# Optimization experiments

Measured on AMD Instinct MI355X. Metric: run time of the kernel, lower is better.

The kernel has to match this reference:

```python
import jax, jax.numpy as jnp
import numpy as np
from jax import lax

TAU = 1.0  # registered buffer, default 1.0 -> Q_tau = +inf -> clamp is a no-op
EPS = 1e-5
SQRT2 = float(np.sqrt(2.0))

# sign with straight-through estimator (weights): grad = identity
@jax.custom_vjp
def sign_w(w):
    return jnp.sign(w)
def _sign_w_fwd(w):
    return jnp.sign(w), None
def _sign_w_bwd(_, g):
    return (g,)
sign_w.defvjp(_sign_w_fwd, _sign_w_bwd)

@jax.custom_vjp
def sign_a(x):
    return jnp.sign(x)
def _sign_a_fwd(x):
    return jnp.sign(x), x
def _sign_a_bwd(x, g):
    return (jnp.maximum(2.0 - jnp.abs(2.0 * x), 0.0) * g,)
sign_a.defvjp(_sign_a_fwd, _sign_a_bwd)

def binarize_conv2d(a, w, alpha, stride=1):
    # weight standardization (torch.var is unbiased -> ddof=1)
    w0 = w - jnp.mean(w, axis=(1, 2, 3), keepdims=True)
    var = jnp.var(w0, axis=(1, 2, 3), keepdims=True, ddof=1)
    w1 = w0 * (2.0 * SQRT2) / jnp.sqrt(var + EPS)
    EW = jnp.mean(jnp.abs(w1))
    Q_tau = lax.stop_gradient(-EW * jnp.log(2.0 - 2.0 * TAU))  # +inf for tau=1
    w2 = jnp.clip(w1, -Q_tau, Q_tau)
    bw = sign_w(w2)
    ba = sign_a(a)  # eval mode: a0 = a (no per-sample var normalization)
    out = lax.conv_general_dilated(
        ba, bw, window_strides=(stride, stride), padding=((1, 1), (1, 1)),
        dimension_numbers=('NCHW', 'OIHW', 'NCHW'))
    return out * alpha[None]  # alpha: [C_out,1,1] -> broadcast over N,H,W

def bn_eval(x, gamma, beta, mean, var):
    scale = (gamma / jnp.sqrt(var + EPS)).reshape(1, -1, 1, 1)
    shift = (beta - mean * gamma / jnp.sqrt(var + EPS)).reshape(1, -1, 1, 1)
    return x * scale + shift

def hardtanh(x):
    return jnp.clip(x, -1.0, 1.0)

def setup_inputs() -> dict:
    key = jax.random.key(0)
    ks = jax.random.split(key, 13)
    N, C, H, W = 64, 256, 32, 32
    return {
        'x': jax.random.normal(ks[0], (N, C, H, W), jnp.float32),
        'conv1_w': jax.random.normal(ks[1], (C, C, 3, 3), jnp.float32) * 0.05,
        'alpha1': jax.random.uniform(ks[2], (C, 1, 1), jnp.float32),
        'bn1_gamma': jax.random.uniform(ks[3], (C,), jnp.float32) + 0.5,
        'bn1_beta': jax.random.normal(ks[4], (C,), jnp.float32) * 0.1,
        'bn1_mean': jax.random.normal(ks[5], (C,), jnp.float32),
        'bn1_var': jax.random.uniform(ks[6], (C,), jnp.float32) + 0.5,
        'conv2_w': jax.random.normal(ks[7], (C, C, 3, 3), jnp.float32) * 0.05,
        'alpha2': jax.random.uniform(ks[8], (C, 1, 1), jnp.float32),
        'bn2_gamma': jax.random.uniform(ks[9], (C,), jnp.float32) + 0.5,
        'bn2_beta': jax.random.normal(ks[10], (C,), jnp.float32) * 0.1,
        'bn2_mean': jax.random.normal(ks[11], (C,), jnp.float32),
        'bn2_var': jax.random.uniform(ks[12], (C,), jnp.float32) + 0.5,
    }

def reference(x, conv1_w, alpha1, bn1_gamma, bn1_beta, bn1_mean, bn1_var,
              conv2_w, alpha2, bn2_gamma, bn2_beta, bn2_mean, bn2_var):
    out = hardtanh(bn_eval(binarize_conv2d(x, conv1_w, alpha1, stride=1),
                           bn1_gamma, bn1_beta, bn1_mean, bn1_var))
    out = bn_eval(binarize_conv2d(out, conv2_w, alpha2, stride=1),
                  bn2_gamma, bn2_beta, bn2_mean, bn2_var)
    out = out + x  # identity shortcut (stride=1, in_planes==planes)
    return hardtanh(out)
```

## Files before the change

### kernel.cpp

```cpp
#include <hip/hip_runtime.h>
#include <cstdint>
#include <cstddef>

using u32 = unsigned int;
using u64 = unsigned long long;

typedef int v4i  __attribute__((ext_vector_type(4)));
typedef int v16i __attribute__((ext_vector_type(16)));

#define EPSV 1e-5f
#define MFMA_I8(A, B, C) __builtin_amdgcn_mfma_i32_32x32x32_i8((A), (B), (C), 0, 0, 0)

__global__ void prep_weights(const float* __restrict__ w1, const float* __restrict__ w2,
                             const float* __restrict__ a1, const float* __restrict__ g1,
                             const float* __restrict__ b1, const float* __restrict__ m1,
                             const float* __restrict__ v1,
                             const float* __restrict__ a2, const float* __restrict__ g2,
                             const float* __restrict__ b2, const float* __restrict__ m2,
                             const float* __restrict__ v2,
                             unsigned char* __restrict__ Wsgn, float4* __restrict__ SC4)
{
    const int co   = blockIdx.x;
    const int conv = blockIdx.y;
    const int c    = threadIdx.x;
    const float* w = conv ? w2 : w1;

    float wv[9];
    const float* wp = w + ((size_t)co * 256 + c) * 9;
    float s = 0.f;
#pragma unroll
    for (int p = 0; p < 9; ++p) { wv[p] = wp[p]; s += wv[p]; }

    __shared__ float red[256];
    red[c] = s;
    __syncthreads();
    for (int off = 128; off > 0; off >>= 1) {
        if (c < off) red[c] += red[c + off];
        __syncthreads();
    }
    const float mean = __fdiv_rn(red[0], 2304.0f);

    unsigned char* wrow = Wsgn + ((size_t)(conv * 256 + co) * 9) * 256;
#pragma unroll
    for (int p = 0; p < 9; ++p)
        wrow[p * 256 + c] = (wv[p] > mean) ? 0x01u : 0xFFu;

    if (c == 0) {
        const float alpha = conv ? a2[co] : a1[co];
        const float gamma = conv ? g2[co] : g1[co];
        const float beta  = conv ? b2[co] : b1[co];
        const float mu    = conv ? m2[co] : m1[co];
        const float var   = conv ? v2[co] : v1[co];
        const float sq    = __fsqrt_rn(__fadd_rn(var, EPSV));
        const float scale = __fdiv_rn(gamma, sq);
        const float shift = __fsub_rn(beta, __fdiv_rn(__fmul_rn(mu, gamma), sq));
        SC4[conv * 256 + co] = make_float4(alpha, scale, shift, 0.f);
    }
}

__global__ void build_bfrag(const unsigned char* __restrict__ Wsgn, uint4* __restrict__ Bf)
{
    const int f    = blockIdx.x;
    const int lane = threadIdx.x;
    const int conv = f / 576;
    const int rem  = f % 576;
    const int g    = rem / 72;
    const int p    = (rem % 72) / 8;
    const int cb   = rem % 8;
    const int co   = g * 32 + (lane & 31);
    const unsigned char* src = Wsgn + ((size_t)(conv * 256 + co) * 9 + p) * 256
                                    + cb * 32 + (lane >> 5) * 16;
    Bf[(size_t)f * 64 + lane] = *(const uint4*)src;
}

__global__ void binarize_x(const float* __restrict__ x, u32* __restrict__ A1)
{
    const int n = blockIdx.x >> 3;
    const int j = blockIdx.x & 7;
    const int p = threadIdx.x;
    const float* xp = x + (((size_t)n * 256 + j * 32) * 1024) + p;
    u32 bits = 0;
#pragma unroll
    for (int k = 0; k < 32; ++k) {
        float v = xp[(size_t)k * 1024];
        bits |= (v > 0.f ? 1u : 0u) << k;
    }
    A1[((size_t)n * 1024 + p) * 8 + j] = bits;
}

__device__ __forceinline__ u32 expand4(u32 x)
{
    u32 r;
    r  = ((x & 1u) ? 0x00000001u : 0x000000FFu);
    r |= ((x & 2u) ? 0x00000100u : 0x0000FF00u);
    r |= ((x & 4u) ? 0x00010000u : 0x00FF0000u);
    r |= ((x & 8u) ? 0x01000000u : 0xFF000000u);
    return r;
}

__device__ __forceinline__ void glds16(const void* g, void* l)
{
    __builtin_amdgcn_global_load_lds(
        (const __attribute__((address_space(1))) void*)g,
        (__attribute__((address_space(3))) void*)l, 16, 0, 0);
}

template<int CONV>
__global__ __launch_bounds__(512, 2)
void conv_mfma(const u32* __restrict__ A_in, const v4i* __restrict__ Bf,
               const float4* __restrict__ SC4, const float* __restrict__ X,
               u32* __restrict__ A_out, float* __restrict__ OUT)
{
    const int n    = blockIdx.x >> 2;
    const int yo   = blockIdx.x & 3;
    const int y0   = yo * 8;
    const int tid  = threadIdx.x;
    const int wave = tid >> 6;
    const int lane = tid & 63;
    const int wm   = wave >> 2;
    const int wn   = wave & 3;
    const int col0 = lane & 31;
    const int g0   = wn * 2;

    __shared__ alignas(16) unsigned char lds[103424];

    const int fbias = (CONV == 2) ? 576 : 0;
    const char* bsrcA = (const char*)Bf + (((size_t)(fbias + g0 * 72)) << 10)
                        + (size_t)lane * 16;
    const char* bsrcB = bsrcA + (72u << 10);
    unsigned char* bdst = lds + 87040 + (size_t)g0 * 1024;

    glds16(bsrcA,        bdst);
    glds16(bsrcB,        bdst + 1024);
    glds16(bsrcA + 1024, bdst + 8192);
    glds16(bsrcB + 1024, bdst + 8192 + 1024);

    for (int s = tid; s < 5440; s += 512) {
        const int colv = s % 34;
        const int rest = s / 34;
        const int r    = rest % 10;
        const int c16  = rest / 10;
        const int iy   = y0 - 1 + r;
        const int ix   = colv - 1;
        u32 d0 = 0, d1 = 0, d2 = 0, d3 = 0;
        if ((unsigned)iy < 32u && (unsigned)ix < 32u) {
            const u32 wrd = A_in[((size_t)n * 1024 + iy * 32 + ix) * 8 + (c16 >> 1)];
            const u32 h = (wrd >> ((c16 & 1) * 16)) & 0xFFFFu;
            d0 = expand4(h);
            d1 = expand4(h >> 4);
            d2 = expand4(h >> 8);
            d3 = expand4(h >> 12);
        }
        *(uint4*)(lds + (size_t)s * 16) = make_uint4(d0, d1, d2, d3);
    }

    const int bias2 = (CONV == 2) ? 256 : 0;
    const float4 scA = SC4[bias2 + (g0 + 0) * 32 + col0];
    const float4 scB = SC4[bias2 + (g0 + 1) * 32 + col0];

    __syncthreads();

    const v16i Z  = {0,0,0,0,0,0,0,0,0,0,0,0,0,0,0,0};
    v16i c0a = Z, c0b = Z, c1a = Z, c1b = Z;
    v16i c2a = Z, c2b = Z, c3a = Z, c3b = Z;

    const u32 lc16off = (u32)((lane >> 5) * 5440);
    const u32 rowbase = (u32)((4 * wm) * 544);
    const u32 bwoff   = (u32)(g0 * 1024 + lane * 16);

    v4i ea0, ea1, ea2, ea3, eb0, eb1;
    v4i oa0, oa1, oa2, oa3, ob0, ob1;
    {
        const u32 ao = lc16off + rowbase + (u32)(col0 * 16);
        ea0 = *(const v4i*)(lds + ao);
        ea1 = *(const v4i*)(lds + ao + 544);
        ea2 = *(const v4i*)(lds + ao + 1088);
        ea3 = *(const v4i*)(lds + ao + 1632);
        const u32 bo = 87040u + bwoff;
        eb0 = *(const v4i*)(lds + bo);
        eb1 = *(const v4i*)(lds + bo + 1024);
    }

#define PHASE(KC, AN0, AN1, AN2, AN3, BN0, BN1, AC0, AC1, AC2, AC3, BC0, BC1)   \
    {                                                                           \
        const int k_ = (KC);                                                    \
        int kf_ = k_ + 2; if (kf_ >= 72) kf_ -= 72;                             \
        {                                                                       \
            unsigned char* d_ = bdst + ((k_ & 1) << 13);                        \
            glds16(bsrcA + ((size_t)kf_ << 10), d_);                            \
            glds16(bsrcB + ((size_t)kf_ << 10), d_ + 1024);                     \
        }                                                                       \
        __builtin_amdgcn_sched_barrier(0);                                      \
        {                                                                       \
            const int kn_ = k_ + 1;                                             \
            const int cb_ = kn_ & 7, p_ = kn_ >> 3;                             \
            const int dy_ = p_ / 3, dx_ = p_ - dy_ * 3;                         \
            const u32 ao_ = lc16off + (u32)(2 * cb_) * 5440u + rowbase          \
                          + (u32)(dy_ * 544) + (u32)((dx_ + col0) * 16);        \
            AN0 = *(const v4i*)(lds + ao_);                                     \
            AN1 = *(const v4i*)(lds + ao_ + 544);                               \
            AN2 = *(const v4i*)(lds + ao_ + 1088);                              \
            AN3 = *(const v4i*)(lds + ao_ + 1632);                              \
            asm volatile("s_waitcnt vmcnt(2)" ::: "memory");                    \
            __builtin_amdgcn_sched_barrier(0);                                  \
            const u32 bo_ = 87040u + (u32)((kn_ & 1) << 13) + bwoff;            \
            BN0 = *(const v4i*)(lds + bo_);                                     \
            BN1 = *(const v4i*)(lds + bo_ + 1024);                              \
        }                                                                       \
        __builtin_amdgcn_s_barrier();                                           \
        asm volatile("s_waitcnt lgkmcnt(6)" ::: "memory");                      \
        __builtin_amdgcn_sched_barrier(0);                                      \
        __builtin_amdgcn_s_setprio(1);                                          \
        c0a = MFMA_I8(AC0, BC0, c0a);  c0b = MFMA_I8(AC0, BC1, c0b);            \
        c1a = MFMA_I8(AC1, BC0, c1a);  c1b = MFMA_I8(AC1, BC1, c1b);            \
        c2a = MFMA_I8(AC2, BC0, c2a);  c2b = MFMA_I8(AC2, BC1, c2b);            \
        c3a = MFMA_I8(AC3, BC0, c3a);  c3b = MFMA_I8(AC3, BC1, c3b);            \
        __builtin_amdgcn_s_setprio(0);                                          \
        __builtin_amdgcn_s_barrier();                                           \
    }

#pragma unroll 1
    for (int j = 0; j < 36; ++j) {
        const int k = j * 2;
        PHASE(k,     oa0, oa1, oa2, oa3, ob0, ob1,  ea0, ea1, ea2, ea3, eb0, eb1)
        PHASE(k + 1, ea0, ea1, ea2, ea3, eb0, eb1,  oa0, oa1, oa2, oa3, ob0, ob1)
    }
#undef PHASE

    if (CONV == 1) {
#define EP1(ACC, MR, GI, SC)                                                    \
        { _Pragma("unroll")                                                     \
          for (int reg = 0; reg < 16; ++reg) {                                  \
              const float t = __fadd_rn(__fmul_rn(__fmul_rn((float)ACC[reg],    \
                                        SC.x), SC.y), SC.z);                    \
              const u64 m = __ballot(t > 0.f);                                  \
              if (lane == 0) {                                                  \
                  const int x = (reg & 3) + 8 * (reg >> 2);                     \
                  const int row = y0 + 4 * wm + (MR);                           \
                  const size_t pb = (size_t)n * 1024 + row * 32 + x;            \
                  A_out[pb * 8 + (g0 + (GI))]       = (u32)m;                   \
                  A_out[(pb + 4) * 8 + (g0 + (GI))] = (u32)(m >> 32);           \
              } } }
        EP1(c0a, 0, 0, scA)  EP1(c0b, 0, 1, scB)
        EP1(c1a, 1, 0, scA)  EP1(c1b, 1, 1, scB)
        EP1(c2a, 2, 0, scA)  EP1(c2b, 2, 1, scB)
        EP1(c3a, 3, 0, scA)  EP1(c3b, 3, 1, scB)
#undef EP1
    } else {
        __syncthreads();
        float* ep = (float*)lds;
#define EP2PASS(CA, CB, R)                                                      \
        { if (wm == ((R) >> 2)) {                                               \
            _Pragma("unroll")                                                   \
            for (int reg = 0; reg < 16; ++reg) {                                \
                const int x = (reg & 3) + 8 * (reg >> 2) + 4 * (lane >> 5);     \
                ep[x * 257 + (g0 + 0) * 32 + col0] =                            \
                    __fadd_rn(__fmul_rn(__fmul_rn((float)CA[reg], scA.x),       \
                                        scA.y), scA.z);                         \
                ep[x * 257 + (g0 + 1) * 32 + col0] =                            \
                    __fadd_rn(__fmul_rn(__fmul_rn((float)CB[reg], scB.x),       \
                                        scB.y), scB.z);                         \
            } }                                                                 \
          __syncthreads();                                                      \
          {                                                                     \
              const int co = tid >> 1, xh = tid & 1;                            \
              const size_t gb = ((size_t)(n * 256 + co)) * 1024                 \
                              + (y0 + (R)) * 32 + xh * 16;                      \
              _Pragma("unroll")                                                 \
              for (int x4 = 0; x4 < 16; x4 += 4) {                              \
                  float4 rr;                                                    \
                  rr.x = ep[(xh * 16 + x4 + 0) * 257 + co];                     \
                  rr.y = ep[(xh * 16 + x4 + 1) * 257 + co];                     \
                  rr.z = ep[(xh * 16 + x4 + 2) * 257 + co];                     \
                  rr.w = ep[(xh * 16 + x4 + 3) * 257 + co];                     \
                  const float4 xv = *(const float4*)(X + gb + x4);              \
                  rr.x = fminf(1.f, fmaxf(-1.f, __fadd_rn(rr.x, xv.x)));        \
                  rr.y = fminf(1.f, fmaxf(-1.f, __fadd_rn(rr.y, xv.y)));        \
                  rr.z = fminf(1.f, fmaxf(-1.f, __fadd_rn(rr.z, xv.z)));        \
                  rr.w = fminf(1.f, fmaxf(-1.f, __fadd_rn(rr.w, xv.w)));        \
                  *(float4*)(OUT + gb + x4) = rr;                               \
              }                                                                 \
          }                                                                     \
          __syncthreads(); }
        EP2PASS(c0a, c0b, 0)
        EP2PASS(c1a, c1b, 1)
        EP2PASS(c2a, c2b, 2)
        EP2PASS(c3a, c3b, 3)
        EP2PASS(c0a, c0b, 4)
        EP2PASS(c1a, c1b, 5)
        EP2PASS(c2a, c2b, 6)
        EP2PASS(c3a, c3b, 7)
#undef EP2PASS
    }
}

extern "C" void kernel_launch(void* const* d_in, const int* in_sizes, int n_in,
                              void* d_out, int out_size, void* d_ws, size_t ws_size,
                              hipStream_t stream)
{
    const float* x   = (const float*)d_in[0];
    const float* w1  = (const float*)d_in[1];
    const float* al1 = (const float*)d_in[2];
    const float* g1  = (const float*)d_in[3];
    const float* b1  = (const float*)d_in[4];
    const float* m1  = (const float*)d_in[5];
    const float* v1  = (const float*)d_in[6];
    const float* w2  = (const float*)d_in[7];
    const float* al2 = (const float*)d_in[8];
    const float* g2  = (const float*)d_in[9];
    const float* b2  = (const float*)d_in[10];
    const float* m2  = (const float*)d_in[11];
    const float* v2  = (const float*)d_in[12];
    float* out = (float*)d_out;

    char* ws = (char*)d_ws;
    float4*        SC4  = (float4*)(ws);
    unsigned char* Wsgn = (unsigned char*)(ws + (64u << 10));
    uint4*         Bf   = (uint4*)(ws + (2u << 20));
    u32*           A1   = (u32*)(ws + (4u << 20));
    u32*           A2   = (u32*)(ws + (6u << 20));
    (void)ws_size; (void)in_sizes; (void)n_in; (void)out_size;

    prep_weights<<<dim3(256, 2), 256, 0, stream>>>(w1, w2, al1, g1, b1, m1, v1,
                                                   al2, g2, b2, m2, v2, Wsgn, SC4);
    build_bfrag<<<dim3(1152), 64, 0, stream>>>(Wsgn, Bf);
    binarize_x<<<dim3(512), 1024, 0, stream>>>(x, A1);
    conv_mfma<1><<<dim3(256), 512, 0, stream>>>(A1, (const v4i*)Bf, SC4,
                                                nullptr, A2, nullptr);
    conv_mfma<2><<<dim3(256), 512, 0, stream>>>(A2, (const v4i*)Bf, SC4,
                                                x, nullptr, out);
}
```

Baseline: 129.9 us.

## Use 4 waves with 4x4 MFMA tiles per wave and per-wave B pipeline

```diff
diff --git a/kernel.cpp b/kernel.cpp
--- a/kernel.cpp
+++ b/kernel.cpp
@@ -106,7 +106,7 @@
 }
 
 template<int CONV>
-__global__ __launch_bounds__(512, 2)
+__global__ __launch_bounds__(256, 1)
 void conv_mfma(const u32* __restrict__ A_in, const v4i* __restrict__ Bf,
                const float4* __restrict__ SC4, const float* __restrict__ X,
                u32* __restrict__ A_out, float* __restrict__ OUT)
@@ -117,25 +117,30 @@
     const int tid  = threadIdx.x;
     const int wave = tid >> 6;
     const int lane = tid & 63;
-    const int wm   = wave >> 2;
-    const int wn   = wave & 3;
+    const int wm   = wave >> 1;
+    const int wn   = wave & 1;
     const int col0 = lane & 31;
-    const int g0   = wn * 2;
-
-    __shared__ alignas(16) unsigned char lds[103424];
+    const int g0   = wn * 4;
+
+    __shared__ alignas(16) unsigned char lds[152576];
 
     const int fbias = (CONV == 2) ? 576 : 0;
-    const char* bsrcA = (const char*)Bf + (((size_t)(fbias + g0 * 72)) << 10)
-                        + (size_t)lane * 16;
-    const char* bsrcB = bsrcA + (72u << 10);
-    unsigned char* bdst = lds + 87040 + (size_t)g0 * 1024;
-
-    glds16(bsrcA,        bdst);
-    glds16(bsrcB,        bdst + 1024);
-    glds16(bsrcA + 1024, bdst + 8192);
-    glds16(bsrcB + 1024, bdst + 8192 + 1024);
-
-    for (int s = tid; s < 5440; s += 512) {
+    const char* bs0 = (const char*)Bf + (((size_t)(fbias + (g0 + 0) * 72)) << 10) + (size_t)lane * 16;
+    const char* bs1 = (const char*)Bf + (((size_t)(fbias + (g0 + 1) * 72)) << 10) + (size_t)lane * 16;
+    const char* bs2 = (const char*)Bf + (((size_t)(fbias + (g0 + 2) * 72)) << 10) + (size_t)lane * 16;
+    const char* bs3 = (const char*)Bf + (((size_t)(fbias + (g0 + 3) * 72)) << 10) + (size_t)lane * 16;
+    unsigned char* bdst = lds + 87040 + (size_t)wave * 16384;
+
+#pragma unroll
+    for (int s = 0; s < 3; ++s) {
+        unsigned char* d = bdst + s * 4096;
+        glds16(bs0 + ((size_t)s << 10), d);
+        glds16(bs1 + ((size_t)s << 10), d + 1024);
+        glds16(bs2 + ((size_t)s << 10), d + 2048);
+        glds16(bs3 + ((size_t)s << 10), d + 3072);
+    }
+
+    for (int s = tid; s < 5440; s += 256) {
         const int colv = s % 34;
         const int rest = s / 34;
         const int r    = rest % 10;
@@ -157,78 +162,92 @@
     const int bias2 = (CONV == 2) ? 256 : 0;
     const float4 scA = SC4[bias2 + (g0 + 0) * 32 + col0];
     const float4 scB = SC4[bias2 + (g0 + 1) * 32 + col0];
+    const float4 scC = SC4[bias2 + (g0 + 2) * 32 + col0];
+    const float4 scD = SC4[bias2 + (g0 + 3) * 32 + col0];
 
     __syncthreads();
 
     const v16i Z  = {0,0,0,0,0,0,0,0,0,0,0,0,0,0,0,0};
-    v16i c0a = Z, c0b = Z, c1a = Z, c1b = Z;
-    v16i c2a = Z, c2b = Z, c3a = Z, c3b = Z;
-
-    const u32 lc16off = (u32)((lane >> 5) * 5440);
-    const u32 rowbase = (u32)((4 * wm) * 544);
-    const u32 bwoff   = (u32)(g0 * 1024 + lane * 16);
-
-    v4i ea0, ea1, ea2, ea3, eb0, eb1;
-    v4i oa0, oa1, oa2, oa3, ob0, ob1;
+    v16i c00 = Z, c01 = Z, c02 = Z, c03 = Z;
+    v16i c10 = Z, c11 = Z, c12 = Z, c13 = Z;
+    v16i c20 = Z, c21 = Z, c22 = Z, c23 = Z;
+    v16i c30 = Z, c31 = Z, c32 = Z, c33 = Z;
+
+    const u32 lhalf = (u32)((lane >> 5) * 5440);
+    const u32 bb    = 87040u + (u32)(wave * 16384 + lane * 16);
+
+    v4i ea0, ea1, ea2, ea3, eb0, eb1, eb2, eb3;
+    v4i oa0, oa1, oa2, oa3, ob0, ob1, ob2, ob3;
     {
-        const u32 ao = lc16off + rowbase + (u32)(col0 * 16);
+        const u32 ao = (lhalf + (u32)((4 * wm) * 544 + col0 * 16)) * 16u / 16u;
         ea0 = *(const v4i*)(lds + ao);
+        ea1 = *(const v4i*)(lds + ao + 544 * 16 / 16 * 1 + 544 - 544 + 544);
         ea1 = *(const v4i*)(lds + ao + 544);
         ea2 = *(const v4i*)(lds + ao + 1088);
         ea3 = *(const v4i*)(lds + ao + 1632);
-        const u32 bo = 87040u + bwoff;
-        eb0 = *(const v4i*)(lds + bo);
-        eb1 = *(const v4i*)(lds + bo + 1024);
-    }
-
-#define PHASE(KC, AN0, AN1, AN2, AN3, BN0, BN1, AC0, AC1, AC2, AC3, BC0, BC1)   \
+        eb0 = *(const v4i*)(lds + bb);
+        eb1 = *(const v4i*)(lds + bb + 1024);
+        eb2 = *(const v4i*)(lds + bb + 2048);
+        eb3 = *(const v4i*)(lds + bb + 3072);
+    }
+
+#define SB __builtin_amdgcn_sched_barrier(0)
+
+#define STEP(KC, A0,A1,A2,A3, B0,B1,B2,B3, NA0,NA1,NA2,NA3, NB0,NB1,NB2,NB3)    \
     {                                                                           \
         const int k_ = (KC);                                                    \
-        int kf_ = k_ + 2; if (kf_ >= 72) kf_ -= 72;                             \
-        {                                                                       \
-            unsigned char* d_ = bdst + ((k_ & 1) << 13);                        \
-            glds16(bsrcA + ((size_t)kf_ << 10), d_);                            \
-            glds16(bsrcB + ((size_t)kf_ << 10), d_ + 1024);                     \
+        asm volatile("s_waitcnt lgkmcnt(0)" ::: "memory");                      \
+        SB;                                                                     \
+        {    \
+            int kg = k_ + 3; if (kg >= 72) kg -= 72;                            \
+            unsigned char* d_ = bdst + ((k_ + 3) & 3) * 4096;                   \
+            glds16(bs0 + ((size_t)kg << 10), d_);                               \
+            glds16(bs1 + ((size_t)kg << 10), d_ + 1024);                        \
+            glds16(bs2 + ((size_t)kg << 10), d_ + 2048);                        \
+            glds16(bs3 + ((size_t)kg << 10), d_ + 3072);                        \
         }                                                                       \
-        __builtin_amdgcn_sched_barrier(0);                                      \
-        {                                                                       \
-            const int kn_ = k_ + 1;                                             \
-            const int cb_ = kn_ & 7, p_ = kn_ >> 3;                             \
-            const int dy_ = p_ / 3, dx_ = p_ - dy_ * 3;                         \
-            const u32 ao_ = lc16off + (u32)(2 * cb_) * 5440u + rowbase          \
-                          + (u32)(dy_ * 544) + (u32)((dx_ + col0) * 16);        \
-            AN0 = *(const v4i*)(lds + ao_);                                     \
-            AN1 = *(const v4i*)(lds + ao_ + 544);                               \
-            AN2 = *(const v4i*)(lds + ao_ + 1088);                              \
-            AN3 = *(const v4i*)(lds + ao_ + 1632);                              \
-            asm volatile("s_waitcnt vmcnt(2)" ::: "memory");                    \
-            __builtin_amdgcn_sched_barrier(0);                                  \
-            const u32 bo_ = 87040u + (u32)((kn_ & 1) << 13) + bwoff;            \
-            BN0 = *(const v4i*)(lds + bo_);                                     \
-            BN1 = *(const v4i*)(lds + bo_ + 1024);                              \
-        }                                                                       \
-        __builtin_amdgcn_s_barrier();                                           \
-        asm volatile("s_waitcnt lgkmcnt(6)" ::: "memory");                      \
-        __builtin_amdgcn_sched_barrier(0);                                      \
-        __builtin_amdgcn_s_setprio(1);                                          \
-        c0a = MFMA_I8(AC0, BC0, c0a);  c0b = MFMA_I8(AC0, BC1, c0b);            \
-        c1a = MFMA_I8(AC1, BC0, c1a);  c1b = MFMA_I8(AC1, BC1, c1b);            \
-        c2a = MFMA_I8(AC2, BC0, c2a);  c2b = MFMA_I8(AC2, BC1, c2b);            \
-        c3a = MFMA_I8(AC3, BC0, c3a);  c3b = MFMA_I8(AC3, BC1, c3b);            \
-        __builtin_amdgcn_s_setprio(0);                                          \
-        __builtin_amdgcn_s_barrier();                                           \
+        SB;                                                                     \
+        const int kn_ = k_ + 1;                                                 \
+        const int cbn_ = kn_ & 7, pn_ = kn_ >> 3;                               \
+        const int dyn_ = (pn_ * 11) >> 5;                                       \
+        const int dxn_ = pn_ - dyn_ * 3;                                        \
+        const u32 aon_ = lhalf + (u32)(cbn_ * 10880)                            \
+                       + (u32)((4 * wm + dyn_) * 544)                          \
+                       + (u32)((col0 + dxn_) * 16);                            \
+        const u32 bon_ = bb + (u32)((kn_ & 3) * 4096);                          \
+        NA0 = *(const v4i*)(lds + aon_);                                        \
+        c00 = MFMA_I8(A0, B0, c00);  c01 = MFMA_I8(A0, B1, c01);  SB;           \
+        NA1 = *(const v4i*)(lds + aon_ + 544);                                  \
+        c02 = MFMA_I8(A0, B2, c02);  c03 = MFMA_I8(A0, B3, c03);  SB;           \
+        NA2 = *(const v4i*)(lds + aon_ + 1088);                                 \
+        c10 = MFMA_I8(A1, B0, c10);  c11 = MFMA_I8(A1, B1, c11);  SB;           \
+        NA3 = *(const v4i*)(lds + aon_ + 1632);                                 \
+        c12 = MFMA_I8(A1, B2, c12);  c13 = MFMA_I8(A1, B3, c13);  SB;           \
+        asm volatile("s_waitcnt vmcnt(8)" ::: "memory");                        \
+        SB;                                                                     \
+        NB0 = *(const v4i*)(lds + bon_);                                        \
+        c20 = MFMA_I8(A2, B0, c20);  c21 = MFMA_I8(A2, B1, c21);  SB;           \
+        NB1 = *(const v4i*)(lds + bon_ + 1024);                                 \
+        c22 = MFMA_I8(A2, B2, c22);  c23 = MFMA_I8(A2, B3, c23);  SB;           \
+        NB2 = *(const v4i*)(lds + bon_ + 2048);                                 \
+        c30 = MFMA_I8(A3, B0, c30);  c31 = MFMA_I8(A3, B1, c31);  SB;           \
+        NB3 = *(const v4i*)(lds + bon_ + 3072);                                 \
+        c32 = MFMA_I8(A3, B2, c32);  c33 = MFMA_I8(A3, B3, c33);  SB;           \
     }
 
 #pragma unroll 1
     for (int j = 0; j < 36; ++j) {
         const int k = j * 2;
-        PHASE(k,     oa0, oa1, oa2, oa3, ob0, ob1,  ea0, ea1, ea2, ea3, eb0, eb1)
-        PHASE(k + 1, ea0, ea1, ea2, ea3, eb0, eb1,  oa0, oa1, oa2, oa3, ob0, ob1)
-    }
-#undef PHASE
+        STEP(k,     ea0,ea1,ea2,ea3, eb0,eb1,eb2,eb3,
+                    oa0,oa1,oa2,oa3, ob0,ob1,ob2,ob3)
+        STEP(k + 1, oa0,oa1,oa2,oa3, ob0,ob1,ob2,ob3,
+                    ea0,ea1,ea2,ea3, eb0,eb1,eb2,eb3)
+    }
+#undef STEP
+#undef SB
 
     if (CONV == 1) {
-#define EP1(ACC, MR, GI, SC)                                                    \
+#define EP1(ACC, RI, GI, SC)                                                    \
         { _Pragma("unroll")                                                     \
           for (int reg = 0; reg < 16; ++reg) {                                  \
               const float t = __fadd_rn(__fmul_rn(__fmul_rn((float)ACC[reg],    \
@@ -236,20 +255,20 @@
               const u64 m = __ballot(t > 0.f);                                  \
               if (lane == 0) {                                                  \
                   const int x = (reg & 3) + 8 * (reg >> 2);                     \
-                  const int row = y0 + 4 * wm + (MR);                           \
+                  const int row = y0 + 4 * wm + (RI);                           \
                   const size_t pb = (size_t)n * 1024 + row * 32 + x;            \
                   A_out[pb * 8 + (g0 + (GI))]       = (u32)m;                   \
                   A_out[(pb + 4) * 8 + (g0 + (GI))] = (u32)(m >> 32);           \
               } } }
-        EP1(c0a, 0, 0, scA)  EP1(c0b, 0, 1, scB)
-        EP1(c1a, 1, 0, scA)  EP1(c1b, 1, 1, scB)
-        EP1(c2a, 2, 0, scA)  EP1(c2b, 2, 1, scB)
-        EP1(c3a, 3, 0, scA)  EP1(c3b, 3, 1, scB)
+        EP1(c00, 0, 0, scA)  EP1(c01, 0, 1, scB)  EP1(c02, 0, 2, scC)  EP1(c03, 0, 3, scD)
+        EP1(c10, 1, 0, scA)  EP1(c11, 1, 1, scB)  EP1(c12, 1, 2, scC)  EP1(c13, 1, 3, scD)
+        EP1(c20, 2, 0, scA)  EP1(c21, 2, 1, scB)  EP1(c22, 2, 2, scC)  EP1(c23, 2, 3, scD)
+        EP1(c30, 3, 0, scA)  EP1(c31, 3, 1, scB)  EP1(c32, 3, 2, scC)  EP1(c33, 3, 3, scD)
 #undef EP1
     } else {
         __syncthreads();
         float* ep = (float*)lds;
-#define EP2PASS(CA, CB, R)                                                      \
+#define EP2PASS(CA, CB, CC, CD, R)                                              \
         { if (wm == ((R) >> 2)) {                                               \
             _Pragma("unroll")                                                   \
             for (int reg = 0; reg < 16; ++reg) {                                \
@@ -260,19 +279,25 @@
                 ep[x * 257 + (g0 + 1) * 32 + col0] =                            \
                     __fadd_rn(__fmul_rn(__fmul_rn((float)CB[reg], scB.x),       \
                                         scB.y), scB.z);                         \
+                ep[x * 257 + (g0 + 2) * 32 + col0] =                            \
+                    __fadd_rn(__fmul_rn(__fmul_rn((float)CC[reg], scC.x),       \
+                                        scC.y), scC.z);                         \
+                ep[x * 257 + (g0 + 3) * 32 + col0] =                            \
+                    __fadd_rn(__fmul_rn(__fmul_rn((float)CD[reg], scD.x),       \
+                                        scD.y), scD.z);                         \
             } }                                                                 \
           __syncthreads();                                                      \
           {                                                                     \
-              const int co = tid >> 1, xh = tid & 1;                            \
+              const int co = tid;                                               \
               const size_t gb = ((size_t)(n * 256 + co)) * 1024                 \
-                              + (y0 + (R)) * 32 + xh * 16;                      \
+                              + (y0 + (R)) * 32;                                \
               _Pragma("unroll")                                                 \
-              for (int x4 = 0; x4 < 16; x4 += 4) {                              \
+              for (int x4 = 0; x4 < 32; x4 += 4) {                              \
                   float4 rr;                                                    \
-                  rr.x = ep[(xh * 16 + x4 + 0) * 257 + co];                     \
-                  rr.y = ep[(xh * 16 + x4 + 1) * 257 + co];                     \
-                  rr.z = ep[(xh * 16 + x4 + 2) * 257 + co];                     \
-                  rr.w = ep[(xh * 16 + x4 + 3) * 257 + co];                     \
+                  rr.x = ep[(x4 + 0) * 257 + co];                               \
+                  rr.y = ep[(x4 + 1) * 257 + co];                               \
+                  rr.z = ep[(x4 + 2) * 257 + co];                               \
+                  rr.w = ep[(x4 + 3) * 257 + co];                               \
                   const float4 xv = *(const float4*)(X + gb + x4);              \
                   rr.x = fminf(1.f, fmaxf(-1.f, __fadd_rn(rr.x, xv.x)));        \
                   rr.y = fminf(1.f, fmaxf(-1.f, __fadd_rn(rr.y, xv.y)));        \
@@ -282,14 +307,14 @@
               }                                                                 \
           }                                                                     \
           __syncthreads(); }
-        EP2PASS(c0a, c0b, 0)
-        EP2PASS(c1a, c1b, 1)
-        EP2PASS(c2a, c2b, 2)
-        EP2PASS(c3a, c3b, 3)
-        EP2PASS(c0a, c0b, 4)
-        EP2PASS(c1a, c1b, 5)
-        EP2PASS(c2a, c2b, 6)
-        EP2PASS(c3a, c3b, 7)
+        EP2PASS(c00, c01, c02, c03, 0)
+        EP2PASS(c10, c11, c12, c13, 1)
+        EP2PASS(c20, c21, c22, c23, 2)
+        EP2PASS(c30, c31, c32, c33, 3)
+        EP2PASS(c00, c01, c02, c03, 4)
+        EP2PASS(c10, c11, c12, c13, 5)
+        EP2PASS(c20, c21, c22, c23, 6)
+        EP2PASS(c30, c31, c32, c33, 7)
 #undef EP2PASS
     }
 }
@@ -325,8 +350,8 @@
                                                    al2, g2, b2, m2, v2, Wsgn, SC4);
     build_bfrag<<<dim3(1152), 64, 0, stream>>>(Wsgn, Bf);
     binarize_x<<<dim3(512), 1024, 0, stream>>>(x, A1);
-    conv_mfma<1><<<dim3(256), 512, 0, stream>>>(A1, (const v4i*)Bf, SC4,
+    conv_mfma<1><<<dim3(256), 256, 0, stream>>>(A1, (const v4i*)Bf, SC4,
                                                 nullptr, A2, nullptr);
-    conv_mfma<2><<<dim3(256), 512, 0, stream>>>(A2, (const v4i*)Bf, SC4,
+    conv_mfma<2><<<dim3(256), 256, 0, stream>>>(A2, (const v4i*)Bf, SC4,
                                                 x, nullptr, out);
 }
```

Result: slower. 310.5 us (+139.2%).

## Process two K-steps per barrier phase with a 4-deep weight ring and XCD block swizzle

Applied to the files above, without the earlier changes.

```diff
diff --git a/kernel.cpp b/kernel.cpp
--- a/kernel.cpp
+++ b/kernel.cpp
@@ -111,8 +111,9 @@
                const float4* __restrict__ SC4, const float* __restrict__ X,
                u32* __restrict__ A_out, float* __restrict__ OUT)
 {
-    const int n    = blockIdx.x >> 2;
-    const int yo   = blockIdx.x & 3;
+    const int logical = (blockIdx.x & 7) * 32 + (blockIdx.x >> 3);
+    const int n    = logical >> 2;
+    const int yo   = logical & 3;
     const int y0   = yo * 8;
     const int tid  = threadIdx.x;
     const int wave = tid >> 6;
@@ -122,18 +123,23 @@
     const int col0 = lane & 31;
     const int g0   = wn * 2;
 
-    __shared__ alignas(16) unsigned char lds[103424];
+    __shared__ alignas(16) unsigned char lds[152576];
 
     const int fbias = (CONV == 2) ? 576 : 0;
     const char* bsrcA = (const char*)Bf + (((size_t)(fbias + g0 * 72)) << 10)
                         + (size_t)lane * 16;
     const char* bsrcB = bsrcA + (72u << 10);
-    unsigned char* bdst = lds + 87040 + (size_t)g0 * 1024;
-
-    glds16(bsrcA,        bdst);
-    glds16(bsrcB,        bdst + 1024);
-    glds16(bsrcA + 1024, bdst + 8192);
-    glds16(bsrcB + 1024, bdst + 8192 + 1024);
+
+#pragma unroll
+    for (int pf = 0; pf < 2; ++pf) {
+        unsigned char* d = lds + 87040 + pf * 16384 + wn * 4096;
+        const size_t k0 = (size_t)(2 * pf) << 10;
+        const size_t k1 = (size_t)(2 * pf + 1) << 10;
+        glds16(bsrcA + k0, d);
+        glds16(bsrcB + k0, d + 1024);
+        glds16(bsrcA + k1, d + 2048);
+        glds16(bsrcB + k1, d + 3072);
+    }
 
     for (int s = tid; s < 5440; s += 512) {
         const int colv = s % 34;
@@ -164,66 +170,90 @@
     v16i c0a = Z, c0b = Z, c1a = Z, c1b = Z;
     v16i c2a = Z, c2b = Z, c3a = Z, c3b = Z;
 
-    const u32 lc16off = (u32)((lane >> 5) * 5440);
+    const u32 lhalf   = (u32)((lane >> 5) * 5440);
     const u32 rowbase = (u32)((4 * wm) * 544);
-    const u32 bwoff   = (u32)(g0 * 1024 + lane * 16);
-
-    v4i ea0, ea1, ea2, ea3, eb0, eb1;
-    v4i oa0, oa1, oa2, oa3, ob0, ob1;
+    const u32 bwoff   = (u32)(wn * 4096 + lane * 16);
+
+    v4i ea0, ea1, ea2, ea3, ea4, ea5, ea6, ea7;
+    v4i oa0, oa1, oa2, oa3, oa4, oa5, oa6, oa7;
     {
-        const u32 ao = lc16off + rowbase + (u32)(col0 * 16);
-        ea0 = *(const v4i*)(lds + ao);
-        ea1 = *(const v4i*)(lds + ao + 544);
-        ea2 = *(const v4i*)(lds + ao + 1088);
-        ea3 = *(const v4i*)(lds + ao + 1632);
-        const u32 bo = 87040u + bwoff;
-        eb0 = *(const v4i*)(lds + bo);
-        eb1 = *(const v4i*)(lds + bo + 1024);
-    }
-
-#define PHASE(KC, AN0, AN1, AN2, AN3, BN0, BN1, AC0, AC1, AC2, AC3, BC0, BC1)   \
+        const u32 a0 = lhalf + rowbase + (u32)(col0 * 16);
+        ea0 = *(const v4i*)(lds + a0);
+        ea1 = *(const v4i*)(lds + a0 + 544);
+        ea2 = *(const v4i*)(lds + a0 + 1088);
+        ea3 = *(const v4i*)(lds + a0 + 1632);
+        const u32 a1 = a0 + 10880;
+        ea4 = *(const v4i*)(lds + a1);
+        ea5 = *(const v4i*)(lds + a1 + 544);
+        ea6 = *(const v4i*)(lds + a1 + 1088);
+        ea7 = *(const v4i*)(lds + a1 + 1632);
+    }
+
+#define PHASE(PH, AC0,AC1,AC2,AC3,AC4,AC5,AC6,AC7,                              \
+                  AN0,AN1,AN2,AN3,AN4,AN5,AN6,AN7)                              \
     {                                                                           \
-        const int k_ = (KC);                                                    \
-        int kf_ = k_ + 2; if (kf_ >= 72) kf_ -= 72;                             \
-        {                                                                       \
-            unsigned char* d_ = bdst + ((k_ & 1) << 13);                        \
-            glds16(bsrcA + ((size_t)kf_ << 10), d_);                            \
-            glds16(bsrcB + ((size_t)kf_ << 10), d_ + 1024);                     \
+        const int ph_ = (PH);                                                   \
+        {     \
+            int pf_ = ph_ + 2; if (pf_ >= 36) pf_ -= 36;                        \
+            unsigned char* d_ = lds + 87040 + ((ph_ + 2) & 3) * 16384           \
+                              + wn * 4096;                                      \
+            const size_t k0_ = (size_t)(2 * pf_) << 10;                         \
+            const size_t k1_ = (size_t)(2 * pf_ + 1) << 10;                     \
+            glds16(bsrcA + k0_, d_);                                            \
+            glds16(bsrcB + k0_, d_ + 1024);                                     \
+            glds16(bsrcA + k1_, d_ + 2048);                                     \
+            glds16(bsrcB + k1_, d_ + 3072);                                     \
         }                                                                       \
+        asm volatile("s_waitcnt vmcnt(8)" ::: "memory");                        \
         __builtin_amdgcn_sched_barrier(0);                                      \
-        {                                                                       \
-            const int kn_ = k_ + 1;                                             \
-            const int cb_ = kn_ & 7, p_ = kn_ >> 3;                             \
-            const int dy_ = p_ / 3, dx_ = p_ - dy_ * 3;                         \
-            const u32 ao_ = lc16off + (u32)(2 * cb_) * 5440u + rowbase          \
-                          + (u32)(dy_ * 544) + (u32)((dx_ + col0) * 16);        \
-            AN0 = *(const v4i*)(lds + ao_);                                     \
-            AN1 = *(const v4i*)(lds + ao_ + 544);                               \
-            AN2 = *(const v4i*)(lds + ao_ + 1088);                              \
-            AN3 = *(const v4i*)(lds + ao_ + 1632);                              \
-            asm volatile("s_waitcnt vmcnt(2)" ::: "memory");                    \
-            __builtin_amdgcn_sched_barrier(0);                                  \
-            const u32 bo_ = 87040u + (u32)((kn_ & 1) << 13) + bwoff;            \
-            BN0 = *(const v4i*)(lds + bo_);                                     \
-            BN1 = *(const v4i*)(lds + bo_ + 1024);                              \
+        const u32 bo_ = 87040u + (u32)((ph_ & 3) * 16384) + bwoff;              \
+        const v4i bk0g0_ = *(const v4i*)(lds + bo_);                            \
+        const v4i bk0g1_ = *(const v4i*)(lds + bo_ + 1024);                     \
+        const v4i bk1g0_ = *(const v4i*)(lds + bo_ + 2048);                     \
+        const v4i bk1g1_ = *(const v4i*)(lds + bo_ + 3072);                     \
+        {                                     \
+            const int ka_ = 2 * ph_ + 2;                                        \
+            const int cb0_ = ka_ & 7, p0_ = ka_ >> 3;                           \
+            const int dy0_ = p0_ / 3, dx0_ = p0_ - dy0_ * 3;                    \
+            const u32 ao0_ = lhalf + (u32)(cb0_ * 10880) + rowbase              \
+                           + (u32)(dy0_ * 544) + (u32)((dx0_ + col0) * 16);     \
+            AN0 = *(const v4i*)(lds + ao0_);                                    \
+            AN1 = *(const v4i*)(lds + ao0_ + 544);                              \
+            AN2 = *(const v4i*)(lds + ao0_ + 1088);                             \
+            AN3 = *(const v4i*)(lds + ao0_ + 1632);                             \
+            const int kb_ = ka_ + 1;                                            \
+            const int cb1_ = kb_ & 7, p1_ = kb_ >> 3;                           \
+            const int dy1_ = p1_ / 3, dx1_ = p1_ - dy1_ * 3;                    \
+            const u32 ao1_ = lhalf + (u32)(cb1_ * 10880) + rowbase              \
+                           + (u32)(dy1_ * 544) + (u32)((dx1_ + col0) * 16);     \
+            AN4 = *(const v4i*)(lds + ao1_);                                    \
+            AN5 = *(const v4i*)(lds + ao1_ + 544);                              \
+            AN6 = *(const v4i*)(lds + ao1_ + 1088);                             \
+            AN7 = *(const v4i*)(lds + ao1_ + 1632);                             \
         }                                                                       \
         __builtin_amdgcn_s_barrier();                                           \
-        asm volatile("s_waitcnt lgkmcnt(6)" ::: "memory");                      \
+        asm volatile("s_waitcnt lgkmcnt(8)" ::: "memory");                      \
         __builtin_amdgcn_sched_barrier(0);                                      \
         __builtin_amdgcn_s_setprio(1);                                          \
-        c0a = MFMA_I8(AC0, BC0, c0a);  c0b = MFMA_I8(AC0, BC1, c0b);            \
-        c1a = MFMA_I8(AC1, BC0, c1a);  c1b = MFMA_I8(AC1, BC1, c1b);            \
-        c2a = MFMA_I8(AC2, BC0, c2a);  c2b = MFMA_I8(AC2, BC1, c2b);            \
-        c3a = MFMA_I8(AC3, BC0, c3a);  c3b = MFMA_I8(AC3, BC1, c3b);            \
+        c0a = MFMA_I8(AC0, bk0g0_, c0a);  c0b = MFMA_I8(AC0, bk0g1_, c0b);      \
+        c1a = MFMA_I8(AC1, bk0g0_, c1a);  c1b = MFMA_I8(AC1, bk0g1_, c1b);      \
+        c2a = MFMA_I8(AC2, bk0g0_, c2a);  c2b = MFMA_I8(AC2, bk0g1_, c2b);      \
+        c3a = MFMA_I8(AC3, bk0g0_, c3a);  c3b = MFMA_I8(AC3, bk0g1_, c3b);      \
+        c0a = MFMA_I8(AC4, bk1g0_, c0a);  c0b = MFMA_I8(AC4, bk1g1_, c0b);      \
+        c1a = MFMA_I8(AC5, bk1g0_, c1a);  c1b = MFMA_I8(AC5, bk1g1_, c1b);      \
+        c2a = MFMA_I8(AC6, bk1g0_, c2a);  c2b = MFMA_I8(AC6, bk1g1_, c2b);      \
+        c3a = MFMA_I8(AC7, bk1g0_, c3a);  c3b = MFMA_I8(AC7, bk1g1_, c3b);      \
         __builtin_amdgcn_s_setprio(0);                                          \
         __builtin_amdgcn_s_barrier();                                           \
     }
 
 #pragma unroll 1
-    for (int j = 0; j < 36; ++j) {
-        const int k = j * 2;
-        PHASE(k,     oa0, oa1, oa2, oa3, ob0, ob1,  ea0, ea1, ea2, ea3, eb0, eb1)
-        PHASE(k + 1, ea0, ea1, ea2, ea3, eb0, eb1,  oa0, oa1, oa2, oa3, ob0, ob1)
+    for (int j = 0; j < 18; ++j) {
+        const int ph = j * 2;
+        PHASE(ph,     ea0,ea1,ea2,ea3,ea4,ea5,ea6,ea7,
+                      oa0,oa1,oa2,oa3,oa4,oa5,oa6,oa7)
+        PHASE(ph + 1, oa0,oa1,oa2,oa3,oa4,oa5,oa6,oa7,
+                      ea0,ea1,ea2,ea3,ea4,ea5,ea6,ea7)
     }
 #undef PHASE
 
```

Result: no change. 129.4 us (-0.3%).
